# Kernel tuning notes

Hardware: AMD Instinct MI355X
Metric: run time of the kernel (lower is better)

The kernel has to match this reference:

```python
import jax, jax.numpy as jnp
import numpy as np

V, H, L, B, S = 32000, 1024, 2, 8, 256


def setup_inputs() -> dict:
    key = jax.random.key(0)
    ks = jax.random.split(key, 12)
    s = 1.0 / np.sqrt(H)  # PyTorch LSTM/Linear init range
    u = lambda k, shape: jax.random.uniform(k, shape, jnp.float32, -s, s)
    return {
        "x": jax.random.randint(ks[0], (B, S), 0, V, dtype=jnp.int32),
        "h0": jnp.zeros((L, B, H), jnp.float32),
        "c0": jnp.zeros((L, B, H), jnp.float32),
        "w_ih0": u(ks[1], (4 * H, V)),
        "w_hh0": u(ks[2], (4 * H, H)),
        "b_ih0": u(ks[3], (4 * H,)),
        "b_hh0": u(ks[4], (4 * H,)),
        "w_ih1": u(ks[5], (4 * H, H)),
        "w_hh1": u(ks[6], (4 * H, H)),
        "b_ih1": u(ks[7], (4 * H,)),
        "b_hh1": u(ks[8], (4 * H,)),
        "fc_w": u(ks[9], (V, H)),
        "fc_b": u(ks[10], (V,)),
    }


def _lstm_layer(xproj, h0, c0, w_hh):
    """xproj: [S,B,4H] input-to-gate projection (biases folded in).
    Gate order i,f,g,o matches PyTorch."""
    def step(carry, xp):
        h, c = carry
        g = xp + h @ w_hh.T  # [B,4H]
        i, f, gg, o = jnp.split(g, 4, axis=-1)
        c = jax.nn.sigmoid(f) * c + jax.nn.sigmoid(i) * jnp.tanh(gg)
        h = jax.nn.sigmoid(o) * jnp.tanh(c)
        return (h, c), h
    (hT, cT), hs = jax.lax.scan(step, (h0, c0), xproj)
    return hs, hT, cT


def reference(x, h0, c0, w_ih0, w_hh0, b_ih0, b_hh0, w_ih1, w_hh1, b_ih1, b_hh1, fc_w, fc_b):
    # F.one_hot(x, V).float() @ w_ih0.T  ==  gather of rows of w_ih0.T (identical math)
    xp0 = jnp.take(w_ih0.T, x, axis=0) + (b_ih0 + b_hh0)  # [B,S,4H]
    xp0 = xp0.transpose(1, 0, 2)  # [S,B,4H] for time-major scan
    h1s, h1T, c1T = _lstm_layer(xp0, h0[0], c0[0], w_hh0)
    xp1 = h1s @ w_ih1.T + (b_ih1 + b_hh1)  # [S,B,4H]
    h2s, h2T, c2T = _lstm_layer(xp1, h0[1], c0[1], w_hh1)
    out = h2s.transpose(1, 0, 2).reshape(-1, H)  # [B*S,H]
    logits = out @ fc_w.T + fc_b  # [B*S,V]
    hn = jnp.stack([h1T, h2T])
    cn = jnp.stack([c1T, c2T])
    return logits, (hn, cn)
```

## Files before the change

### kernel.cpp

```cpp
#include <hip/hip_runtime.h>
#include <cmath>

typedef float  f32x4  __attribute__((ext_vector_type(4)));
typedef float  f32x2  __attribute__((ext_vector_type(2)));
typedef __bf16 bf16x8 __attribute__((ext_vector_type(8)));

static constexpr int HN  = 1024;
static constexpr int VN  = 32000;
static constexpr int BN  = 8;
static constexpr int SN  = 256;
static constexpr int H4N = 4096;

__global__ __launch_bounds__(256) void k_gather(const int* __restrict__ x,
    const float* __restrict__ w_ih0, const float* __restrict__ b_ih0,
    const float* __restrict__ b_hh0, float* __restrict__ xpB) {
  int t = blockIdx.x;
  __shared__ int toks[8];
  if (threadIdx.x < 8) toks[threadIdx.x] = x[threadIdx.x * SN + t];
  __syncthreads();
  int wgx = threadIdx.x;
  for (int g = 0; g < 4; ++g) {
    float vals[4][8];
    #pragma unroll
    for (int u = 0; u < 4; ++u) {
      int row = g * 1024 + wgx * 4 + u;
      float bias = b_ih0[row] + b_hh0[row];
      const float* wr = w_ih0 + (size_t)row * VN;
      #pragma unroll
      for (int b = 0; b < 8; ++b) vals[u][b] = wr[toks[b]] + bias;
    }
    float* dst = xpB + (((size_t)t * 256 + wgx) * 16 + g * 4) * 8;
    #pragma unroll
    for (int u = 0; u < 4; ++u) {
      *(f32x4*)&dst[u * 8]     = *(f32x4*)&vals[u][0];
      *(f32x4*)&dst[u * 8 + 4] = *(f32x4*)&vals[u][4];
    }
  }
}

__global__ __launch_bounds__(256, 1) void k_lstm(
    const float* __restrict__ xpB,
    const float* __restrict__ w_hh,
    const float* __restrict__ h0,
    const float* __restrict__ c0,
    float* __restrict__ hs,
    float* __restrict__ hn, float* __restrict__ cn) {
  __shared__ float wL[16][1024];
  __shared__ float hL[8192];
  __shared__ float red[8][4][4][32];
  __shared__ float gates[16][8];

  const int tid = threadIdx.x;
  const int wg  = blockIdx.x;
  const int u0  = wg * 4;

  for (int it = 0; it < 16; ++it) {
    int g = it >> 2, u = it & 3;
    int k4 = tid;
    int k4s = k4 ^ ((k4 >> 3) & 7);
    f32x4 v = *(const f32x4*)&w_hh[((size_t)g * HN + u0 + u) * HN + k4 * 4];
    *(f32x4*)&wL[it][k4s * 4] = v;
  }
  float c_reg = 0.f;
  if (tid < 32) c_reg = c0[(tid & 7) * HN + u0 + (tid >> 3)];

  const int ks = tid & 31, rg = (tid >> 5) & 3, bg = tid >> 7;
  const int ksx = ks & 7;
  const int hb = tid & 7;
  const int hk = tid >> 3;
  const int prow = tid >> 3, pb = tid & 7;
  __syncthreads();

  for (int t = 0; t < SN; ++t) {
    float xpv = 0.f;
    if (tid < 128)
      xpv = xpB[(((size_t)t * 256 + wg) * 16 + prow) * 8 + pb];

    unsigned long long rv[16];
    if (t == 0) {
      const unsigned long long* s8 =
          (const unsigned long long*)h0 + (size_t)hb * 512 + hk;
      #pragma unroll
      for (int j = 0; j < 16; ++j) rv[j] = s8[j * 32];
    } else {
      const unsigned long long* s8 =
          (const unsigned long long*)(hs + (size_t)(t - 1) * (BN * HN))
          + (size_t)hb * 512 + hk;
      while (true) {
        #pragma unroll
        for (int j = 0; j < 16; ++j)
          rv[j] = __hip_atomic_load((unsigned long long*)(s8 + j * 32),
                                    __ATOMIC_RELAXED, __HIP_MEMORY_SCOPE_AGENT);
        unsigned bad = 0u;
        #pragma unroll
        for (int j = 0; j < 16; ++j) {
          bad |= (unsigned)((unsigned)rv[j] == 0xFFFFFFFFu);
          bad |= (unsigned)((unsigned)(rv[j] >> 32) == 0xFFFFFFFFu);
        }
        if (!bad) break;
        __builtin_amdgcn_s_sleep(1);
      }
    }
    #pragma unroll
    for (int j = 0; j < 16; ++j) {
      int k64 = hk + j * 32;
      int k4 = k64 >> 1, half = k64 & 1;
      int idx = ((k4 << 3) | hb) ^ ((k4 >> 3) & 7);
      *(f32x2*)&hL[idx * 4 + half * 2] = __builtin_bit_cast(f32x2, rv[j]);
    }
    __syncthreads();

    float acc[4][4] = {};
    #pragma unroll
    for (int j = 0; j < 8; ++j) {
      int k4 = ks * 8 + j;
      int k4s = k4 ^ ksx;
      f32x4 wv[4], hv[4];
      #pragma unroll
      for (int ri = 0; ri < 4; ++ri)
        wv[ri] = *(const f32x4*)&wL[rg * 4 + ri][k4s * 4];
      #pragma unroll
      for (int bi = 0; bi < 4; ++bi) {
        int idx = ((k4 << 3) | (bg * 4 + bi)) ^ ksx;
        hv[bi] = *(const f32x4*)&hL[idx * 4];
      }
      #pragma unroll
      for (int ri = 0; ri < 4; ++ri)
        #pragma unroll
        for (int bi = 0; bi < 4; ++bi)
          acc[ri][bi] += wv[ri][0]*hv[bi][0] + wv[ri][1]*hv[bi][1]
                       + wv[ri][2]*hv[bi][2] + wv[ri][3]*hv[bi][3];
    }
    #pragma unroll
    for (int ri = 0; ri < 4; ++ri)
      #pragma unroll
      for (int bi = 0; bi < 4; ++bi)
        red[rg * 2 + bg][ri][bi][ks] = acc[ri][bi];
    __syncthreads();

    if (tid < 128) {
      int rrg = prow >> 2, ri = prow & 3, bbg = pb >> 2, bi = pb & 3;
      const float* rp = red[rrg * 2 + bbg][ri][bi];
      float s = 0.f;
      #pragma unroll
      for (int q = 0; q < 32; ++q) s += rp[(q + tid) & 31];
      gates[prow][pb] = s + xpv;
    }
    __syncthreads();

    if (tid < 32) {
      int u = tid >> 3, b = tid & 7;
      float gi = gates[0 * 4 + u][b], gf = gates[1 * 4 + u][b];
      float gg = gates[2 * 4 + u][b], go = gates[3 * 4 + u][b];
      float si = 1.f / (1.f + expf(-gi));
      float sf = 1.f / (1.f + expf(-gf));
      float so = 1.f / (1.f + expf(-go));
      c_reg = sf * c_reg + si * tanhf(gg);
      float h = so * tanhf(c_reg);
      __hip_atomic_store(&hs[(size_t)t * (BN * HN) + b * HN + u0 + u], h,
                         __ATOMIC_RELAXED, __HIP_MEMORY_SCOPE_AGENT);
      if (t == SN - 1) {
        hn[b * HN + u0 + u] = h;
        cn[b * HN + u0 + u] = c_reg;
      }
    }
    __syncthreads();
  }
}

__global__ __launch_bounds__(256) void k_split(const float* __restrict__ src,
    __bf16* __restrict__ hi, __bf16* __restrict__ lo) {
  int i = (blockIdx.x * 256 + threadIdx.x) * 4;
  f32x4 v = *(const f32x4*)&src[i];
  #pragma unroll
  for (int j = 0; j < 4; ++j) {
    __bf16 h = (__bf16)v[j];
    hi[i + j] = h;
    lo[i + j] = (__bf16)(v[j] - (float)h);
  }
}

__global__ __launch_bounds__(256) void k_gemm(const __bf16* __restrict__ Ahi,
    const __bf16* __restrict__ Alo, const float* __restrict__ Bsrc,
    const float* __restrict__ bias1, const float* __restrict__ bias2,
    float* __restrict__ C, int Mt, int N, int mode) {
  __shared__ __bf16 sAh[128][32], sAl[128][32], sBh[128][32], sBl[128][32];
  int bid = blockIdx.x;
  int tn = bid / Mt, tm = bid % Mt;
  int tid = threadIdx.x, lane = tid & 63, wid = tid >> 6;
  int wr = wid >> 1, wc = wid & 1;
  f32x4 acc[4][4] = {};
  const size_t K = 1024;

  for (int kk = 0; kk < 1024; kk += 32) {
    __syncthreads();
    #pragma unroll
    for (int it = 0; it < 2; ++it) {
      int c = it * 256 + tid;
      int r = c >> 2, k8 = (c & 3) * 8;
      size_t ga = (size_t)(tm * 128 + r) * K + kk + k8;
      *(bf16x8*)&sAh[r][k8] = *(const bf16x8*)&Ahi[ga];
      *(bf16x8*)&sAl[r][k8] = *(const bf16x8*)&Alo[ga];
      size_t gb = (size_t)(tn * 128 + r) * K + kk + k8;
      f32x4 x0 = *(const f32x4*)&Bsrc[gb];
      f32x4 x1 = *(const f32x4*)&Bsrc[gb + 4];
      bf16x8 bh, bl;
      #pragma unroll
      for (int j = 0; j < 4; ++j) {
        __bf16 h0 = (__bf16)x0[j]; bh[j]     = h0; bl[j]     = (__bf16)(x0[j] - (float)h0);
        __bf16 h1 = (__bf16)x1[j]; bh[4 + j] = h1; bl[4 + j] = (__bf16)(x1[j] - (float)h1);
      }
      *(bf16x8*)&sBh[r][k8] = bh;
      *(bf16x8*)&sBl[r][k8] = bl;
    }
    __syncthreads();

    int kq = (lane >> 4) * 8;
    bf16x8 ah[4], al[4], bh[4], bl[4];
    #pragma unroll
    for (int i = 0; i < 4; ++i) {
      int ra = wr * 64 + i * 16 + (lane & 15);
      ah[i] = *(const bf16x8*)&sAh[ra][kq];
      al[i] = *(const bf16x8*)&sAl[ra][kq];
      int rb = wc * 64 + i * 16 + (lane & 15);
      bh[i] = *(const bf16x8*)&sBh[rb][kq];
      bl[i] = *(const bf16x8*)&sBl[rb][kq];
    }
    #pragma unroll
    for (int i = 0; i < 4; ++i)
      #pragma unroll
      for (int j = 0; j < 4; ++j) {
        acc[i][j] = __builtin_amdgcn_mfma_f32_16x16x32_bf16(ah[i], bh[j], acc[i][j], 0, 0, 0);
        acc[i][j] = __builtin_amdgcn_mfma_f32_16x16x32_bf16(ah[i], bl[j], acc[i][j], 0, 0, 0);
        acc[i][j] = __builtin_amdgcn_mfma_f32_16x16x32_bf16(al[i], bh[j], acc[i][j], 0, 0, 0);
      }
  }

  #pragma unroll
  for (int j = 0; j < 4; ++j) {
    int gcol = tn * 128 + wc * 64 + j * 16 + (lane & 15);
    float bv = bias1[gcol] + (bias2 ? bias2[gcol] : 0.f);
    #pragma unroll
    for (int i = 0; i < 4; ++i) {
      #pragma unroll
      for (int r = 0; r < 4; ++r) {
        int row = tm * 128 + wr * 64 + i * 16 + ((lane >> 4) << 2) + r;
        float val = acc[i][j][r] + bv;
        if (mode == 2) {
          int t = row >> 3, b = row & 7;
          int g = gcol >> 10, rem = gcol & 1023, wgx = rem >> 2, u = rem & 3;
          C[(((size_t)t * 256 + wgx) * 16 + g * 4 + u) * 8 + b] = val;
        } else {
          int orow = (mode == 1) ? ((row & 7) * 256 + (row >> 3)) : row;
          C[(size_t)orow * N + gcol] = val;
        }
      }
    }
  }
}

extern "C" void kernel_launch(void* const* d_in, const int* in_sizes, int n_in,
                              void* d_out, int out_size, void* d_ws, size_t ws_size,
                              hipStream_t stream) {
  (void)in_sizes; (void)n_in; (void)out_size; (void)ws_size;
  const int*   x     = (const int*)  d_in[0];
  const float* h0    = (const float*)d_in[1];
  const float* c0    = (const float*)d_in[2];
  const float* w_ih0 = (const float*)d_in[3];
  const float* w_hh0 = (const float*)d_in[4];
  const float* b_ih0 = (const float*)d_in[5];
  const float* b_hh0 = (const float*)d_in[6];
  const float* w_ih1 = (const float*)d_in[7];
  const float* w_hh1 = (const float*)d_in[8];
  const float* b_ih1 = (const float*)d_in[9];
  const float* b_hh1 = (const float*)d_in[10];
  const float* fc_w  = (const float*)d_in[11];
  const float* fc_b  = (const float*)d_in[12];
  float* out = (float*)d_out;
  float* ws  = (float*)d_ws;

  float* xpB  = ws;
  float* h1s  = ws + 8388608;
  float* h2s  = ws + 10485760;
  __bf16* Ahi = (__bf16*)(ws + 12582912);
  __bf16* Alo = (__bf16*)(ws + 13631488);

  const size_t LOG = (size_t)2048 * VN;
  float* hn = out + LOG;
  float* cn = out + LOG + 16384;

  hipMemsetAsync(h1s, 0xFF, (size_t)SN * BN * HN * 4, stream);
  hipMemsetAsync(h2s, 0xFF, (size_t)SN * BN * HN * 4, stream);

  k_gather<<<SN, 256, 0, stream>>>(x, w_ih0, b_ih0, b_hh0, xpB);

  k_lstm<<<256, 256, 0, stream>>>(xpB, w_hh0, h0, c0, h1s, hn, cn);

  k_split<<<2048, 256, 0, stream>>>(h1s, Ahi, Alo);
  k_gemm<<<16 * 32, 256, 0, stream>>>(Ahi, Alo, w_ih1, b_ih1, b_hh1, xpB,
                                      16, H4N, 2);

  k_lstm<<<256, 256, 0, stream>>>(xpB, w_hh1, h0 + BN * HN, c0 + BN * HN,
                                  h2s, hn + BN * HN, cn + BN * HN);

  k_split<<<2048, 256, 0, stream>>>(h2s, Ahi, Alo);
  k_gemm<<<16 * 250, 256, 0, stream>>>(Ahi, Alo, fc_w, fc_b, nullptr, out,
                                       16, VN, 1);
}
```

Baseline: 4.425 ms.

## Fuse layer-1 input projection and bf16 split into recurrent LSTM kernels

Each layer-0 LSTM workgroup now computes its slice of the layer-1 input projection (w_ih1 · h) for the previous timestep right after publishing h. This removes the separate projection GEMM. The layer-1 LSTM writes the hi/lo bf16 split of h directly, which removes both k_split kernels. Per-element 0xFF sentinel polling is replaced with atomic arrival counters, which also drops the two large memsets. The trade-off is extra fp32 dot-product work and w_ih1 reads from global memory inside each serial timestep, which may lengthen the recurrence critical path.

```diff
diff --git a/kernel.cpp b/kernel.cpp
--- a/kernel.cpp
+++ b/kernel.cpp
@@ -39,12 +39,18 @@
 }
 
 __global__ __launch_bounds__(256, 1) void k_lstm(
-    const float* __restrict__ xpB,
+    const float* __restrict__ xpB_in,
     const float* __restrict__ w_hh,
+    const float* __restrict__ w_ih1,
+    const float* __restrict__ bi1,
+    const float* __restrict__ bh1,
     const float* __restrict__ h0,
     const float* __restrict__ c0,
     float* __restrict__ hs,
-    float* __restrict__ hn, float* __restrict__ cn) {
+    float* __restrict__ hn, float* __restrict__ cn,
+    unsigned* __restrict__ bar,
+    float* __restrict__ xpB_out,
+    __bf16* __restrict__ Ahi, __bf16* __restrict__ Alo) {
   __shared__ float wL[16][1024];
   __shared__ float hL[8192];
   __shared__ float red[8][4][4][32];
@@ -69,12 +75,30 @@
   const int hb = tid & 7;
   const int hk = tid >> 3;
   const int prow = tid >> 3, pb = tid & 7;
+
+  float bsum1 = 0.f;
+  if (w_ih1 && tid < 128) {
+    int grow = (prow >> 2) * HN + u0 + (prow & 3);
+    bsum1 = bi1[grow] + bh1[grow];
+  }
+  const float* w2base = w_ih1 ?
+      (w_ih1 + ((size_t)rg * HN + u0) * HN) : nullptr;
   __syncthreads();
 
   for (int t = 0; t < SN; ++t) {
     float xpv = 0.f;
     if (tid < 128)
-      xpv = xpB[(((size_t)t * 256 + wg) * 16 + prow) * 8 + pb];
+      xpv = xpB_in[(((size_t)t * 256 + wg) * 16 + prow) * 8 + pb];
+
+    if (t > 0) {
+      if (tid < 64) {
+        unsigned tgt = 4u * (unsigned)t;
+        while (__hip_atomic_load(&bar[tid * 32], __ATOMIC_RELAXED,
+                                 __HIP_MEMORY_SCOPE_AGENT) < tgt)
+          __builtin_amdgcn_s_sleep(1);
+      }
+      __syncthreads();
+    }
 
     unsigned long long rv[16];
     if (t == 0) {
@@ -86,20 +110,10 @@
       const unsigned long long* s8 =
           (const unsigned long long*)(hs + (size_t)(t - 1) * (BN * HN))
           + (size_t)hb * 512 + hk;
-      while (true) {
-        #pragma unroll
-        for (int j = 0; j < 16; ++j)
-          rv[j] = __hip_atomic_load((unsigned long long*)(s8 + j * 32),
-                                    __ATOMIC_RELAXED, __HIP_MEMORY_SCOPE_AGENT);
-        unsigned bad = 0u;
-        #pragma unroll
-        for (int j = 0; j < 16; ++j) {
-          bad |= (unsigned)((unsigned)rv[j] == 0xFFFFFFFFu);
-          bad |= (unsigned)((unsigned)(rv[j] >> 32) == 0xFFFFFFFFu);
-        }
-        if (!bad) break;
-        __builtin_amdgcn_s_sleep(1);
-      }
+      #pragma unroll
+      for (int j = 0; j < 16; ++j)
+        rv[j] = __hip_atomic_load((unsigned long long*)(s8 + j * 32),
+                                  __ATOMIC_RELAXED, __HIP_MEMORY_SCOPE_AGENT);
     }
     #pragma unroll
     for (int j = 0; j < 16; ++j) {
@@ -159,24 +173,122 @@
       float h = so * tanhf(c_reg);
       __hip_atomic_store(&hs[(size_t)t * (BN * HN) + b * HN + u0 + u], h,
                          __ATOMIC_RELAXED, __HIP_MEMORY_SCOPE_AGENT);
+      if (Ahi) {
+        size_t m = (size_t)(t * 8 + b) * HN + u0 + u;
+        __bf16 hh = (__bf16)h;
+        Ahi[m] = hh;
+        Alo[m] = (__bf16)(h - (float)hh);
+      }
       if (t == SN - 1) {
         hn[b * HN + u0 + u] = h;
         cn[b * HN + u0 + u] = c_reg;
       }
     }
-    __syncthreads();
-  }
-}
-
-__global__ __launch_bounds__(256) void k_split(const float* __restrict__ src,
-    __bf16* __restrict__ hi, __bf16* __restrict__ lo) {
-  int i = (blockIdx.x * 256 + threadIdx.x) * 4;
-  f32x4 v = *(const f32x4*)&src[i];
-  #pragma unroll
-  for (int j = 0; j < 4; ++j) {
-    __bf16 h = (__bf16)v[j];
-    hi[i + j] = h;
-    lo[i + j] = (__bf16)(v[j] - (float)h);
+    if (tid == 0) {
+      asm volatile("s_waitcnt vmcnt(0)" ::: "memory");
+      __hip_atomic_fetch_add(&bar[(wg >> 2) * 32], 1u,
+                             __ATOMIC_RELAXED, __HIP_MEMORY_SCOPE_AGENT);
+    }
+
+    if (w_ih1 && t > 0) {
+      float acc2[4][4] = {};
+      #pragma unroll
+      for (int j = 0; j < 8; ++j) {
+        int k4 = ks * 8 + j;
+        f32x4 wv[4], hv[4];
+        #pragma unroll
+        for (int ri = 0; ri < 4; ++ri)
+          wv[ri] = *(const f32x4*)&w2base[(size_t)ri * HN + k4 * 4];
+        #pragma unroll
+        for (int bi = 0; bi < 4; ++bi) {
+          int idx = ((k4 << 3) | (bg * 4 + bi)) ^ ksx;
+          hv[bi] = *(const f32x4*)&hL[idx * 4];
+        }
+        #pragma unroll
+        for (int ri = 0; ri < 4; ++ri)
+          #pragma unroll
+          for (int bi = 0; bi < 4; ++bi)
+            acc2[ri][bi] += wv[ri][0]*hv[bi][0] + wv[ri][1]*hv[bi][1]
+                          + wv[ri][2]*hv[bi][2] + wv[ri][3]*hv[bi][3];
+      }
+      #pragma unroll
+      for (int ri = 0; ri < 4; ++ri)
+        #pragma unroll
+        for (int bi = 0; bi < 4; ++bi)
+          red[rg * 2 + bg][ri][bi][ks] = acc2[ri][bi];
+      __syncthreads();
+      if (tid < 128) {
+        int rrg = prow >> 2, ri = prow & 3, bbg = pb >> 2, bi = pb & 3;
+        const float* rp = red[rrg * 2 + bbg][ri][bi];
+        float s = 0.f;
+        #pragma unroll
+        for (int q = 0; q < 32; ++q) s += rp[(q + tid) & 31];
+        xpB_out[(((size_t)(t - 1) * 256 + wg) * 16 + prow) * 8 + pb] =
+            s + bsum1;
+      }
+    }
+    __syncthreads();
+  }
+
+  if (w_ih1) {
+    if (tid < 64) {
+      unsigned tgt = 4u * (unsigned)SN;
+      while (__hip_atomic_load(&bar[tid * 32], __ATOMIC_RELAXED,
+                               __HIP_MEMORY_SCOPE_AGENT) < tgt)
+        __builtin_amdgcn_s_sleep(1);
+    }
+    __syncthreads();
+    unsigned long long rv[16];
+    const unsigned long long* s8 =
+        (const unsigned long long*)(hs + (size_t)(SN - 1) * (BN * HN))
+        + (size_t)hb * 512 + hk;
+    #pragma unroll
+    for (int j = 0; j < 16; ++j)
+      rv[j] = __hip_atomic_load((unsigned long long*)(s8 + j * 32),
+                                __ATOMIC_RELAXED, __HIP_MEMORY_SCOPE_AGENT);
+    #pragma unroll
+    for (int j = 0; j < 16; ++j) {
+      int k64 = hk + j * 32;
+      int k4 = k64 >> 1, half = k64 & 1;
+      int idx = ((k4 << 3) | hb) ^ ((k4 >> 3) & 7);
+      *(f32x2*)&hL[idx * 4 + half * 2] = __builtin_bit_cast(f32x2, rv[j]);
+    }
+    __syncthreads();
+    float acc2[4][4] = {};
+    #pragma unroll
+    for (int j = 0; j < 8; ++j) {
+      int k4 = ks * 8 + j;
+      f32x4 wv[4], hv[4];
+      #pragma unroll
+      for (int ri = 0; ri < 4; ++ri)
+        wv[ri] = *(const f32x4*)&w2base[(size_t)ri * HN + k4 * 4];
+      #pragma unroll
+      for (int bi = 0; bi < 4; ++bi) {
+        int idx = ((k4 << 3) | (bg * 4 + bi)) ^ ksx;
+        hv[bi] = *(const f32x4*)&hL[idx * 4];
+      }
+      #pragma unroll
+      for (int ri = 0; ri < 4; ++ri)
+        #pragma unroll
+        for (int bi = 0; bi < 4; ++bi)
+          acc2[ri][bi] += wv[ri][0]*hv[bi][0] + wv[ri][1]*hv[bi][1]
+                        + wv[ri][2]*hv[bi][2] + wv[ri][3]*hv[bi][3];
+    }
+    #pragma unroll
+    for (int ri = 0; ri < 4; ++ri)
+      #pragma unroll
+      for (int bi = 0; bi < 4; ++bi)
+        red[rg * 2 + bg][ri][bi][ks] = acc2[ri][bi];
+    __syncthreads();
+    if (tid < 128) {
+      int rrg = prow >> 2, ri = prow & 3, bbg = pb >> 2, bi = pb & 3;
+      const float* rp = red[rrg * 2 + bbg][ri][bi];
+      float s = 0.f;
+      #pragma unroll
+      for (int q = 0; q < 32; ++q) s += rp[(q + tid) & 31];
+      xpB_out[(((size_t)(SN - 1) * 256 + wg) * 16 + prow) * 8 + pb] =
+          s + bsum1;
+    }
   }
 }
 
@@ -246,14 +358,8 @@
       for (int r = 0; r < 4; ++r) {
         int row = tm * 128 + wr * 64 + i * 16 + ((lane >> 4) << 2) + r;
         float val = acc[i][j][r] + bv;
-        if (mode == 2) {
-          int t = row >> 3, b = row & 7;
-          int g = gcol >> 10, rem = gcol & 1023, wgx = rem >> 2, u = rem & 3;
-          C[(((size_t)t * 256 + wgx) * 16 + g * 4 + u) * 8 + b] = val;
-        } else {
-          int orow = (mode == 1) ? ((row & 7) * 256 + (row >> 3)) : row;
-          C[(size_t)orow * N + gcol] = val;
-        }
+        int orow = (mode == 1) ? ((row & 7) * 256 + (row >> 3)) : row;
+        C[(size_t)orow * N + gcol] = val;
       }
     }
   }
@@ -284,26 +390,25 @@
   float* h2s  = ws + 10485760;
   __bf16* Ahi = (__bf16*)(ws + 12582912);
   __bf16* Alo = (__bf16*)(ws + 13631488);
+  unsigned* bar = (unsigned*)(ws + 14680064);
 
   const size_t LOG = (size_t)2048 * VN;
   float* hn = out + LOG;
   float* cn = out + LOG + 16384;
 
-  hipMemsetAsync(h1s, 0xFF, (size_t)SN * BN * HN * 4, stream);
-  hipMemsetAsync(h2s, 0xFF, (size_t)SN * BN * HN * 4, stream);
+  hipMemsetAsync(bar, 0, 4096 * sizeof(unsigned), stream);
 
   k_gather<<<SN, 256, 0, stream>>>(x, w_ih0, b_ih0, b_hh0, xpB);
 
-  k_lstm<<<256, 256, 0, stream>>>(xpB, w_hh0, h0, c0, h1s, hn, cn);
-
-  k_split<<<2048, 256, 0, stream>>>(h1s, Ahi, Alo);
-  k_gemm<<<16 * 32, 256, 0, stream>>>(Ahi, Alo, w_ih1, b_ih1, b_hh1, xpB,
-                                      16, H4N, 2);
-
-  k_lstm<<<256, 256, 0, stream>>>(xpB, w_hh1, h0 + BN * HN, c0 + BN * HN,
-                                  h2s, hn + BN * HN, cn + BN * HN);
-
-  k_split<<<2048, 256, 0, stream>>>(h2s, Ahi, Alo);
+  k_lstm<<<256, 256, 0, stream>>>(xpB, w_hh0, w_ih1, b_ih1, b_hh1,
+                                  h0, c0, h1s, hn, cn, bar,
+                                  xpB, nullptr, nullptr);
+
+  k_lstm<<<256, 256, 0, stream>>>(xpB, w_hh1, nullptr, nullptr, nullptr,
+                                  h0 + BN * HN, c0 + BN * HN,
+                                  h2s, hn + BN * HN, cn + BN * HN,
+                                  bar + 2048, nullptr, Ahi, Alo);
+
   k_gemm<<<16 * 250, 256, 0, stream>>>(Ahi, Alo, fc_w, fc_b, nullptr, out,
                                        16, VN, 1);
 }
```

Measured after the change: 4.638 ms. 4.8% more time.
